# Optimization experiments

Measured on AMD Instinct MI355X. Metric: run time of the kernel, lower is better.

The kernel has to match this reference:

```python
import jax, jax.numpy as jnp
import numpy as np
from jax import lax

K_NN = 16      # neighbors used by compute_knn_distance
ANCHOR_K = 64  # config['anchor_k']


def _knn_dist_vec(pts):
    """compute_knn_distance for one object: mean offset vector to K_NN nearest neighbors.
    pts: (N, 3) -> (N, 3)"""
    sq = jnp.sum(pts * pts, axis=-1)                      # (N,)
    d2 = sq[:, None] + sq[None, :] - 2.0 * (pts @ pts.T)  # (N, N) squared dists
    n = pts.shape[0]
    d2 = d2 + jnp.eye(n, dtype=pts.dtype) * 1e10          # exclude self
    _, idx = lax.top_k(-d2, K_NN)                          # (N, K_NN) nearest indices
    neigh = pts[idx]                                       # (N, K_NN, 3)
    return jnp.mean(neigh - pts[:, None, :], axis=1)       # (N, 3)


def _fps(pts, k):
    """Farthest point sampling for one object. pts: (N, 3) -> (k,) int32 indices."""
    d0 = jnp.sum((pts - pts[0]) ** 2, axis=-1)             # dist to seed point 0

    def step(min_d, _):
        idx = jnp.argmax(min_d)
        d = jnp.sum((pts - pts[idx]) ** 2, axis=-1)
        return jnp.minimum(min_d, d), idx

    _, idxs = lax.scan(step, d0, None, length=k - 1)
    return jnp.concatenate([jnp.zeros((1,), dtype=idxs.dtype), idxs])


def setup_inputs() -> dict:
    key = jax.random.key(0)
    k1, k2, k3, k4 = jax.random.split(key, 4)
    B, N_obj, N_v = 4, 8, 2048
    positions = jax.random.normal(k1, (B, N_obj, N_v, 3), dtype=jnp.float32)
    velocities = jax.random.normal(k2, (B, N_obj, N_v, 3), dtype=jnp.float32)
    physics_params = jax.random.uniform(k3, (B, N_obj, 3), dtype=jnp.float32)
    # reference pose at t=0: nearby but distinct so rel_pos is nontrivial
    ref_positions = positions + 0.05 * jax.random.normal(k4, (B, N_obj, N_v, 3), dtype=jnp.float32)
    return {"positions": positions, "velocities": velocities,
            "physics_params": physics_params, "ref_positions": ref_positions}


def reference(positions, velocities, physics_params, ref_positions):
    B, N_obj, N_v, _ = positions.shape
    flat = positions.reshape(B * N_obj, N_v, 3)

    # pairwise KNN distance feature per point
    dist_vec = jax.vmap(_knn_dist_vec)(flat).reshape(B, N_obj, N_v, 3)

    # iterative FPS anchor sampling (vectorized over all B*N_obj objects)
    anchors = jax.vmap(lambda p: _fps(p, ANCHOR_K))(flat).reshape(B, N_obj, ANCHOR_K)

    rel_pos = positions - ref_positions

    # multi-field gather at anchor indices (torch.gather on dim=2)
    gather = lambda f: jnp.take_along_axis(f, anchors[..., None], axis=2)
    anchor_dist = gather(dist_vec)       # (B, N_obj, K, 3)
    anchor_vel = gather(velocities)      # (B, N_obj, K, 3)
    anchor_rel = gather(rel_pos)         # (B, N_obj, K, 3)

    phys = jnp.broadcast_to(physics_params[:, :, None, :], (B, N_obj, ANCHOR_K, 3))
    query = jnp.concatenate([anchor_dist, anchor_vel, anchor_rel, phys], axis=-1)  # (B, N_obj, K, 12)
    return query
```

## Files before the change

### kernel.cpp

```cpp
#include <hip/hip_runtime.h>
#include <stdint.h>

#define NPTS 2048
#define KNN  16
#define AK   64
#define TPB  256
#define FPT  (NPTS / TPB)
#define KPL  (NPTS / 64)
#define FW   (NPTS / 64)

typedef unsigned long long u64;
typedef unsigned int u32;
#define UMAX 0xFFFFFFFFFFFFFFFFull

__device__ __forceinline__ float sq3(float x, float y, float z) {
    return __fadd_rn(__fadd_rn(__fmul_rn(x, x), __fmul_rn(y, y)), __fmul_rn(z, z));
}

template <int CTRL>
__device__ __forceinline__ u64 dpp64(u64 k) {
    const int lo = __builtin_amdgcn_update_dpp((int)(u32)k, (int)(u32)k,
                                               CTRL, 0xF, 0xF, false);
    const int hi = __builtin_amdgcn_update_dpp((int)(u32)(k >> 32),
                                               (int)(u32)(k >> 32),
                                               CTRL, 0xF, 0xF, false);
    return ((u64)(u32)hi << 32) | (u32)lo;
}

__device__ __forceinline__ void swap16_pair(u64 k, u64& a, u64& b) {
#if __has_builtin(__builtin_amdgcn_permlane16_swap)
    const u32 lo = (u32)k, hi = (u32)(k >> 32);
    const auto rl = __builtin_amdgcn_permlane16_swap(lo, lo, false, false);
    const auto rh = __builtin_amdgcn_permlane16_swap(hi, hi, false, false);
    a = ((u64)(u32)rh[0] << 32) | (u32)rl[0];
    b = ((u64)(u32)rh[1] << 32) | (u32)rl[1];
#else
    a = (u64)__shfl_xor((long long)k, 16, 64);
    b = a;
#endif
}

__device__ __forceinline__ void swap32_pair(u64 k, u64& a, u64& b) {
#if __has_builtin(__builtin_amdgcn_permlane32_swap)
    const u32 lo = (u32)k, hi = (u32)(k >> 32);
    const auto rl = __builtin_amdgcn_permlane32_swap(lo, lo, false, false);
    const auto rh = __builtin_amdgcn_permlane32_swap(hi, hi, false, false);
    a = ((u64)(u32)rh[0] << 32) | (u32)rl[0];
    b = ((u64)(u32)rh[1] << 32) | (u32)rl[1];
#else
    a = (u64)__shfl_xor((long long)k, 32, 64);
    b = a;
#endif
}

__device__ __forceinline__ u64 wave_max64(u64 k) {
    u64 o, a, b;
    o = dpp64<0xB1>(k);  if (o > k) k = o;
    o = dpp64<0x4E>(k);  if (o > k) k = o;
    o = dpp64<0x141>(k); if (o > k) k = o;
    o = dpp64<0x140>(k); if (o > k) k = o;
    swap16_pair(k, a, b); if (a > k) k = a; if (b > k) k = b;
    swap32_pair(k, a, b); if (a > k) k = a; if (b > k) k = b;
    return k;
}

__device__ __forceinline__ u64 wave_min64(u64 k) {
    u64 o, a, b;
    o = dpp64<0xB1>(k);  if (o < k) k = o;
    o = dpp64<0x4E>(k);  if (o < k) k = o;
    o = dpp64<0x141>(k); if (o < k) k = o;
    o = dpp64<0x140>(k); if (o < k) k = o;
    swap16_pair(k, a, b); if (a < k) k = a; if (b < k) k = b;
    swap32_pair(k, a, b); if (a < k) k = a; if (b < k) k = b;
    return k;
}

__global__ __launch_bounds__(64) void fps_kernel(const float* __restrict__ pos,
                                                 int* __restrict__ anchors) {
    const int obj = blockIdx.x;
    const int lane = threadIdx.x & 63;

    __shared__ float4 sP[NPTS];

    const float* pts = pos + (size_t)obj * NPTS * 3;
    float px[FW], py[FW], pz[FW], mind[FW];
    #pragma unroll
    for (int i = 0; i < FW; i++) {
        const int j = lane + i * 64;
        const float x = pts[j * 3 + 0];
        const float y = pts[j * 3 + 1];
        const float z = pts[j * 3 + 2];
        px[i] = x; py[i] = y; pz[i] = z;
        sP[j] = make_float4(x, y, z, 0.f);
    }
    if (lane == 0) anchors[obj * AK + 0] = 0;

    const float ax0 = __shfl(px[0], 0, 64);
    const float ay0 = __shfl(py[0], 0, 64);
    const float az0 = __shfl(pz[0], 0, 64);
    float bv = -1.0f; u32 bj = 0;
    #pragma unroll
    for (int i = 0; i < FW; i++) {
        const float d2 = sq3(__fsub_rn(px[i], ax0), __fsub_rn(py[i], ay0),
                             __fsub_rn(pz[i], az0));
        mind[i] = d2;
        if (d2 > bv) { bv = d2; bj = (u32)(lane + i * 64); }
    }
    u64 key = ((u64)__float_as_uint(bv) << 32) | (u32)(~bj);

    #pragma unroll 1
    for (int s = 1; s < AK; s++) {
        const u64 wk = wave_max64(key);
        const int widx = (int)(~(u32)wk);
        if (lane == 0) anchors[obj * AK + s] = widx;
        if (s == AK - 1) break;

        const float4 c = sP[widx];

        float nbv = -1.0f; u32 nbj = 0;
        #pragma unroll
        for (int i = 0; i < FW; i++) {
            const float d2 = sq3(__fsub_rn(px[i], c.x), __fsub_rn(py[i], c.y),
                                 __fsub_rn(pz[i], c.z));
            const float nm = fminf(mind[i], d2);
            mind[i] = nm;
            if (nm > nbv) { nbv = nm; nbj = (u32)(lane + i * 64); }
        }
        key = ((u64)__float_as_uint(nbv) << 32) | (u32)(~nbj);
    }
}

__global__ __launch_bounds__(TPB) void knn_gather_kernel(
    const float* __restrict__ pos, const float* __restrict__ vel,
    const float* __restrict__ phys, const float* __restrict__ refp,
    const int* __restrict__ anchors, float* __restrict__ out) {
    const int t = threadIdx.x;
    const int wid = t >> 6, lane = t & 63;
    const int g = blockIdx.x * 4 + wid;
    const int obj = g >> 6;

    __shared__ float4 sP[NPTS];
    const float* pts = pos + (size_t)obj * NPTS * 3;
    #pragma unroll
    for (int i = 0; i < FPT; i++) {
        const int j = t + i * TPB;
        const float x = pts[j * 3 + 0];
        const float y = pts[j * 3 + 1];
        const float z = pts[j * 3 + 2];
        sP[j] = make_float4(x, y, z, sq3(x, y, z));
    }
    const int a = anchors[g];
    __syncthreads();

    const float4 ca = sP[a];
    const float ax = ca.x, ay = ca.y, az = ca.z;
    const float sqa = ca.w;

    u64 k[KPL];
    #pragma unroll
    for (int i = 0; i < KPL; i++) {
        const int j = lane + i * 64;
        const float4 p = sP[j];
        const float dot = __fadd_rn(
            __fadd_rn(__fmul_rn(ax, p.x), __fmul_rn(ay, p.y)), __fmul_rn(az, p.z));
        const float d2 = __fsub_rn(__fadd_rn(sqa, p.w), __fmul_rn(2.0f, dot));
        u32 bb = __float_as_uint(d2);
        bb ^= (bb & 0x80000000u) ? 0xFFFFFFFFu : 0x80000000u;
        k[i] = (j == a) ? UMAX : (((u64)bb << 32) | (u32)j);
    }

    u64 c0 = UMAX, c1 = UMAX, c2 = UMAX, c3 = UMAX;
    #pragma unroll
    for (int i = 0; i < KPL; i++) c0 = (k[i] < c0) ? k[i] : c0;
    #pragma unroll
    for (int i = 0; i < KPL; i++) {
        const u64 v = (k[i] > c0) ? k[i] : UMAX; c1 = (v < c1) ? v : c1;
    }
    #pragma unroll
    for (int i = 0; i < KPL; i++) {
        const u64 v = (k[i] > c1) ? k[i] : UMAX; c2 = (v < c2) ? v : c2;
    }
    #pragma unroll
    for (int i = 0; i < KPL; i++) {
        const u64 v = (k[i] > c2) ? k[i] : UMAX; c3 = (v < c3) ? v : c3;
    }

    float accx = 0.f, accy = 0.f, accz = 0.f;
    u64 thr = 0;
    float4 cw;
    {
        const u64 w = wave_min64(c0);
        cw = sP[(int)(u32)w];
        if (c0 == w) { thr = c0; c0 = c1; c1 = c2; c2 = c3; c3 = UMAX; }
    }
    #pragma unroll 1
    for (int r = 1; r < KNN; r++) {
        if (c0 == UMAX) {
            #pragma unroll
            for (int i = 0; i < KPL; i++) {
                const u64 v = (k[i] > thr) ? k[i] : UMAX; c0 = (v < c0) ? v : c0;
            }
            #pragma unroll
            for (int i = 0; i < KPL; i++) {
                const u64 v = (k[i] > c0) ? k[i] : UMAX; c1 = (v < c1) ? v : c1;
            }
            #pragma unroll
            for (int i = 0; i < KPL; i++) {
                const u64 v = (k[i] > c1) ? k[i] : UMAX; c2 = (v < c2) ? v : c2;
            }
            #pragma unroll
            for (int i = 0; i < KPL; i++) {
                const u64 v = (k[i] > c2) ? k[i] : UMAX; c3 = (v < c3) ? v : c3;
            }
        }
        const u64 w = wave_min64(c0);
        const float4 cn = sP[(int)(u32)w];
        accx = __fadd_rn(accx, __fsub_rn(cw.x, ax));
        accy = __fadd_rn(accy, __fsub_rn(cw.y, ay));
        accz = __fadd_rn(accz, __fsub_rn(cw.z, az));
        cw = cn;
        if (c0 == w) {
            thr = c0; c0 = c1; c1 = c2; c2 = c3; c3 = UMAX;
        }
    }
    accx = __fadd_rn(accx, __fsub_rn(cw.x, ax));
    accy = __fadd_rn(accy, __fsub_rn(cw.y, ay));
    accz = __fadd_rn(accz, __fsub_rn(cw.z, az));

    if (lane == 0) {
        float* o = out + (size_t)g * 12;
        o[0] = __fmul_rn(accx, 0.0625f);
        o[1] = __fmul_rn(accy, 0.0625f);
        o[2] = __fmul_rn(accz, 0.0625f);
        const size_t base = (size_t)obj * NPTS * 3 + (size_t)a * 3;
        o[3] = vel[base + 0];
        o[4] = vel[base + 1];
        o[5] = vel[base + 2];
        o[6] = __fsub_rn(pos[base + 0], refp[base + 0]);
        o[7] = __fsub_rn(pos[base + 1], refp[base + 1]);
        o[8] = __fsub_rn(pos[base + 2], refp[base + 2]);
        const float* ph = phys + (size_t)obj * 3;
        o[9]  = ph[0];
        o[10] = ph[1];
        o[11] = ph[2];
    }
}

extern "C" void kernel_launch(void* const* d_in, const int* in_sizes, int n_in,
                              void* d_out, int out_size, void* d_ws, size_t ws_size,
                              hipStream_t stream) {
    const float* pos  = (const float*)d_in[0];
    const float* vel  = (const float*)d_in[1];
    const float* phys = (const float*)d_in[2];
    const float* refp = (const float*)d_in[3];
    float* out = (float*)d_out;

    const int n_obj = in_sizes[2] / 3;
    int* anchors = (int*)d_ws;

    fps_kernel<<<n_obj, 64, 0, stream>>>(pos, anchors);
    knn_gather_kernel<<<n_obj * AK / 4, TPB, 0, stream>>>(pos, vel, phys, refp,
                                                          anchors, out);
}
```

Baseline: 126.1 us.

## Split FPS across four waves per object with shared-memory cross-wave argmax

The farthest-point-sampling kernel moves from one 64-lane wave per object to a 256-thread block, so each thread handles 8 points instead of 32. Each of the 63 iterations does a wave reduction, then a shared-memory exchange of four wave winners with a block barrier, using double-buffered slots so one barrier per step suffices. Anchors are staged in shared memory and written out once at the end. The aim is to cut the serial per-step distance-update latency, at the cost of a __syncthreads and extra shared-memory traffic every iteration.

```diff
diff --git a/kernel.cpp b/kernel.cpp
--- a/kernel.cpp
+++ b/kernel.cpp
@@ -7,7 +7,6 @@
 #define TPB  256
 #define FPT  (NPTS / TPB)
 #define KPL  (NPTS / 64)
-#define FW   (NPTS / 64)
 
 typedef unsigned long long u64;
 typedef unsigned int u32;
@@ -75,59 +74,80 @@
     return k;
 }
 
-__global__ __launch_bounds__(64) void fps_kernel(const float* __restrict__ pos,
-                                                 int* __restrict__ anchors) {
+__global__ __launch_bounds__(TPB) void fps_kernel(const float* __restrict__ pos,
+                                                  int* __restrict__ anchors) {
     const int obj = blockIdx.x;
-    const int lane = threadIdx.x & 63;
+    const int t = threadIdx.x;
+    const int wid = t >> 6, lane = t & 63;
 
     __shared__ float4 sP[NPTS];
+    __shared__ u64 skey[8];
+    __shared__ float4 scrd[8];
+    __shared__ int sAnc[AK];
 
     const float* pts = pos + (size_t)obj * NPTS * 3;
-    float px[FW], py[FW], pz[FW], mind[FW];
-    #pragma unroll
-    for (int i = 0; i < FW; i++) {
-        const int j = lane + i * 64;
+    float px[FPT], py[FPT], pz[FPT], mind[FPT];
+    #pragma unroll
+    for (int i = 0; i < FPT; i++) {
+        const int j = t + i * TPB;
         const float x = pts[j * 3 + 0];
         const float y = pts[j * 3 + 1];
         const float z = pts[j * 3 + 2];
         px[i] = x; py[i] = y; pz[i] = z;
         sP[j] = make_float4(x, y, z, 0.f);
     }
-    if (lane == 0) anchors[obj * AK + 0] = 0;
-
-    const float ax0 = __shfl(px[0], 0, 64);
-    const float ay0 = __shfl(py[0], 0, 64);
-    const float az0 = __shfl(pz[0], 0, 64);
-    float bv = -1.0f; u32 bj = 0;
-    #pragma unroll
-    for (int i = 0; i < FW; i++) {
-        const float d2 = sq3(__fsub_rn(px[i], ax0), __fsub_rn(py[i], ay0),
-                             __fsub_rn(pz[i], az0));
-        mind[i] = d2;
-        if (d2 > bv) { bv = d2; bj = (u32)(lane + i * 64); }
-    }
-    u64 key = ((u64)__float_as_uint(bv) << 32) | (u32)(~bj);
+    if (t == 0) sAnc[0] = 0;
+    __syncthreads();
+
+    u64 key;
+    {
+        const float4 c0 = sP[0];
+        float bv = -1.0f; u32 bj = 0;
+        #pragma unroll
+        for (int i = 0; i < FPT; i++) {
+            const float d2 = sq3(__fsub_rn(px[i], c0.x), __fsub_rn(py[i], c0.y),
+                                 __fsub_rn(pz[i], c0.z));
+            mind[i] = d2;
+            if (d2 > bv) { bv = d2; bj = (u32)(t + i * TPB); }
+        }
+        key = ((u64)__float_as_uint(bv) << 32) | (u32)(~bj);
+    }
 
     #pragma unroll 1
     for (int s = 1; s < AK; s++) {
         const u64 wk = wave_max64(key);
-        const int widx = (int)(~(u32)wk);
-        if (lane == 0) anchors[obj * AK + s] = widx;
+        const int side = (s & 1) * 4;
+        if (lane == 0) {
+            const int widx = (int)(~(u32)wk);
+            skey[side + wid] = wk;
+            scrd[side + wid] = sP[widx];
+        }
+        __syncthreads();
+        u64 ka = skey[side + 0];
+        float4 ca = scrd[side + 0];
+        { const u64 k1 = skey[side + 1]; const float4 q = scrd[side + 1];
+          if (k1 > ka) { ka = k1; ca = q; } }
+        { const u64 k2 = skey[side + 2]; const float4 q = scrd[side + 2];
+          if (k2 > ka) { ka = k2; ca = q; } }
+        { const u64 k3 = skey[side + 3]; const float4 q = scrd[side + 3];
+          if (k3 > ka) { ka = k3; ca = q; } }
+        if (t == 0) sAnc[s] = (int)(~(u32)ka);
         if (s == AK - 1) break;
 
-        const float4 c = sP[widx];
-
-        float nbv = -1.0f; u32 nbj = 0;
+        float bv = -1.0f; u32 bj = 0;
         #pragma unroll
-        for (int i = 0; i < FW; i++) {
-            const float d2 = sq3(__fsub_rn(px[i], c.x), __fsub_rn(py[i], c.y),
-                                 __fsub_rn(pz[i], c.z));
+        for (int i = 0; i < FPT; i++) {
+            const float d2 = sq3(__fsub_rn(px[i], ca.x), __fsub_rn(py[i], ca.y),
+                                 __fsub_rn(pz[i], ca.z));
             const float nm = fminf(mind[i], d2);
             mind[i] = nm;
-            if (nm > nbv) { nbv = nm; nbj = (u32)(lane + i * 64); }
-        }
-        key = ((u64)__float_as_uint(nbv) << 32) | (u32)(~nbj);
-    }
+            if (nm > bv) { bv = nm; bj = (u32)(t + i * TPB); }
+        }
+        key = ((u64)__float_as_uint(bv) << 32) | (u32)(~bj);
+    }
+
+    __syncthreads();
+    if (t < AK) anchors[obj * AK + t] = sAnc[t];
 }
 
 __global__ __launch_bounds__(TPB) void knn_gather_kernel(
@@ -258,7 +278,7 @@
     const int n_obj = in_sizes[2] / 3;
     int* anchors = (int*)d_ws;
 
-    fps_kernel<<<n_obj, 64, 0, stream>>>(pos, anchors);
+    fps_kernel<<<n_obj, TPB, 0, stream>>>(pos, anchors);
     knn_gather_kernel<<<n_obj * AK / 4, TPB, 0, stream>>>(pos, vel, phys, refp,
                                                           anchors, out);
 }
```

After: 110.9 us. 12.0% less time.
